# Kernel optimization log

Hardware: AMD Instinct MI355X
Metric: run time of the kernel (lower is better)

The kernel has to match this reference:

```python
import jax, jax.numpy as jnp
import numpy as np

B, H, S, D = 4, 16, 2048, 64

def setup_inputs() -> dict:
    key = jax.random.key(0)
    kq, kk, kv = jax.random.split(key, 3)
    q = jax.random.normal(kq, (B, H, S, D), dtype=jnp.float32)
    k = jax.random.normal(kk, (B, H, S, D), dtype=jnp.float32)
    v = jax.random.normal(kv, (B, H, S, D), dtype=jnp.float32)
    return {"q": q, "k": k, "v": v}

def reference(q, k, v):
    # Faithful port of TransformerBlock.scaled_dot_product_attention
    # (is_causal=True, mha_dropout=0.0 / eval mode).
    head_dim = q.shape[-1]
    scale = jnp.asarray(head_dim, q.dtype) ** -0.5
    q_len, k_len = q.shape[-2], k.shape[-2]
    # causal additive bias: 0 on/below diagonal, -inf above
    causal = jnp.tril(jnp.ones((q_len, k_len), dtype=bool))
    attn_bias = jnp.where(causal, jnp.asarray(0.0, q.dtype), jnp.asarray(-jnp.inf, q.dtype))
    # [b,h,s,d] x [b,h,t,d] -> [b,h,s,t]
    attn_weights = jnp.einsum('bhsd,bhtd->bhst', q * scale, k) + attn_bias
    attn = jax.nn.softmax(attn_weights, axis=-1)
    out = jnp.einsum('bhst,bhtd->bhsd', attn, v)
    return out
```

## Files before the change

### kernel.cpp

```cpp
#include <hip/hip_runtime.h>
#include <math.h>


#define S_LEN 2048
#define D_DIM 64
#define TK 64
#define NHEAD 64
#define MASKV -30000.0f
#define MINIT 1000.0f
#define DEFER_THR 12.0f
#define MNEG -30000.0f
#define LSTR 72
#define PREP_KBLK 4096

typedef __attribute__((ext_vector_type(8))) short bf16x8;
typedef __attribute__((ext_vector_type(4))) float f32x4;

static __device__ __forceinline__ float fast_exp2(float x) {
#if __has_builtin(__builtin_amdgcn_exp2f)
    return __builtin_amdgcn_exp2f(x);
#else
    float r;
    asm volatile("v_exp_f32 %0, %1\n\ts_nop 1" : "=v"(r) : "v"(x));
    return r;
#endif
}

static __device__ __forceinline__ float fmax3(float a, float b, float c) {
    return fmaxf(fmaxf(a, b), c);
}

static __device__ __forceinline__ unsigned int pack_bf16(float a, float b) {
    union { float f; unsigned int u; } ca, cb;
    ca.f = a; cb.f = b;
    unsigned int ua = ca.u + 0x8000u;
    unsigned int ub = cb.u + 0x8000u;
    return (ua >> 16) | (ub & 0xFFFF0000u);
}

static __device__ __forceinline__ unsigned int pack_bf16_fast(float a, float b) {
#if __has_builtin(__builtin_amdgcn_perm)
    union { float f; unsigned int u; } ca, cb;
    ca.f = a; cb.f = b;
    return __builtin_amdgcn_perm(cb.u + 0x8000u, ca.u + 0x8000u, 0x07060302u);
#else
    return pack_bf16(a, b);
#endif
}

typedef const __attribute__((address_space(1))) unsigned int* gas1_t;
typedef __attribute__((address_space(3))) unsigned int* las3_t;
static __device__ __forceinline__ void stage16(const void* g, void* l) {
    __builtin_amdgcn_global_load_lds((gas1_t)g, (las3_t)l, 16, 0, 0);
}

__global__ __launch_bounds__(256)
void fa_prep(const float* __restrict__ kg, const float* __restrict__ vg,
             unsigned short* __restrict__ kb, unsigned short* __restrict__ vb)
{
    const int tid = threadIdx.x;
    const int bid = blockIdx.x;
    if (bid < PREP_KBLK) {
        const int cid = bid * 256 + tid;
        const int ch  = cid & 7;
        const int row = cid >> 3;
        const int kv  = row & (S_LEN - 1);
        const float4* s = reinterpret_cast<const float4*>(kg + (size_t)row * D_DIM + ch * 8);
        float4 a = s[0], b = s[1];
        uint4 w;
        w.x = pack_bf16(a.x, a.y); w.y = pack_bf16(a.z, a.w);
        w.z = pack_bf16(b.x, b.y); w.w = pack_bf16(b.z, b.w);
        const int dst = ch ^ (kv & 7);
        *reinterpret_cast<uint4*>(kb + (size_t)row * D_DIM + dst * 8) = w;
    } else {
        const int wv   = (bid - PREP_KBLK) * 4 + (tid >> 6);
        const int lane = tid & 63;
        const int kg8  = lane >> 3;
        const int dg   = lane & 7;
        const float* s = vg + ((size_t)wv * TK + kg8 * 8) * D_DIM + dg * 8;
        float va[8][8];
        #pragma unroll
        for (int i = 0; i < 8; ++i) {
            const float4* sp = reinterpret_cast<const float4*>(s + (size_t)i * D_DIM);
            float4 x = sp[0], y = sp[1];
            va[i][0] = x.x; va[i][1] = x.y; va[i][2] = x.z; va[i][3] = x.w;
            va[i][4] = y.x; va[i][5] = y.y; va[i][6] = y.z; va[i][7] = y.w;
        }
        unsigned short* db = vb + (size_t)wv * (TK * D_DIM);
        #pragma unroll
        for (int j = 0; j < 8; ++j) {
            const int d = dg * 8 + j;
            uint4 w;
            w.x = pack_bf16(va[0][j], va[1][j]);
            w.y = pack_bf16(va[2][j], va[3][j]);
            w.z = pack_bf16(va[4][j], va[5][j]);
            w.w = pack_bf16(va[6][j], va[7][j]);
            *reinterpret_cast<uint4*>(db + d * D_DIM + 8 * (kg8 ^ j)) = w;
        }
    }
}

#define SOFTMAX_GROUP(SV, MC, LI, PL)                                          \
    {                                                                          \
        float x0 = fmax3(SV[0][0], SV[0][1], SV[0][2]);                        \
        float x1 = fmax3(SV[0][3], SV[1][0], SV[1][1]);                        \
        float x2 = fmax3(SV[1][2], SV[1][3], SV[2][0]);                        \
        float x3 = fmax3(SV[2][1], SV[2][2], SV[2][3]);                        \
        float x4 = fmax3(SV[3][0], SV[3][1], SV[3][2]);                        \
        float y0 = fmax3(x0, x1, x2);                                          \
        float y1 = fmax3(x3, x4, SV[3][3]);                                    \
        float rm = fmaxf(y0, y1);                                              \
        rm = fmaxf(rm, __shfl_xor(rm, 16, 64));                                \
        rm = fmaxf(rm, __shfl_xor(rm, 32, 64));                                \
        if (__any(rm > DEFER_THR)) {                                           \
            float mx    = fmaxf(rm, 0.f);                                      \
            float alpha = fast_exp2(-mx);                                      \
            LI *= alpha;                                                       \
            _Pragma("unroll")                                                  \
            for (int nc = 0; nc < 4; ++nc)                                     \
                _Pragma("unroll")                                              \
                for (int r = 0; r < 4; ++r) oacc##SV[nc][r] *= alpha;          \
            _Pragma("unroll")                                                  \
            for (int nt = 0; nt < 4; ++nt)                                     \
                _Pragma("unroll")                                              \
                for (int r = 0; r < 4; ++r) SV[nt][r] -= mx;                   \
            _Pragma("unroll")                                                  \
            for (int r = 0; r < 4; ++r) MC[r] -= mx;                           \
        }                                                                      \
        float rs = 0.f;                                                        \
        _Pragma("unroll")                                                      \
        for (int nt = 0; nt < 4; ++nt) {                                       \
            float e0 = fast_exp2(SV[nt][0]);                                   \
            float e1 = fast_exp2(SV[nt][1]);                                   \
            float e2 = fast_exp2(SV[nt][2]);                                   \
            float e3 = fast_exp2(SV[nt][3]);                                   \
            rs += (e0 + e1) + (e2 + e3);                                       \
            uint2 pw;                                                          \
            pw.x = pack_bf16_fast(e0, e1);                                     \
            pw.y = pack_bf16_fast(e2, e3);                                     \
            *reinterpret_cast<uint2*>(PL + ((nt * 32 + quad * 8) ^ swz)) = pw; \
        }                                                                      \
        rs += __shfl_xor(rs, 16, 64);                                          \
        rs += __shfl_xor(rs, 32, 64);                                          \
        LI += rs;                                                              \
    }

__global__ __launch_bounds__(256, 2)
void fa_fwd(const float* __restrict__ qg,
            const unsigned short* __restrict__ kb,
            const unsigned short* __restrict__ vb,
            float* __restrict__ og)
{
    const int head = blockIdx.x;
    const int pr   = blockIdx.y;
    const int tid  = threadIdx.x;
    const int wave = tid >> 6;
    const int lane = tid & 63;
    const int m16  = lane & 15;
    const int quad = lane >> 4;

    __shared__ unsigned short Kl[2][TK * D_DIM];
    __shared__ unsigned short Vt[2][TK * D_DIM];
    __shared__ unsigned short Pl[4][2][16 * TK];

    const size_t hoff = (size_t)head * S_LEN * D_DIM;
    const unsigned short* kbh = kb + hoff;
    const unsigned short* vbh = vb + hoff;
    float* __restrict__ ogh = og + hoff;

    const int swz  = (m16 & 7) << 4;
    const int colA = (quad * 16) ^ swz;
    const int colB = (64 + quad * 16) ^ swz;
    const int rowB = m16 * 128;
    const int sgo  = wave * 512 + lane * 8;

    char* klds = (char*)&Kl[0][0];
    char* vlds = (char*)&Vt[0][0];
    char* plA  = (char*)&Pl[0][0][0] + wave * 4096 + m16 * 128;
    char* plB  = plA + 2048;
    char* kw   = klds + wave * 1024;
    char* vw   = vlds + wave * 1024;

    const float QSC = 0.18033688011112042f;

    for (int pass = 0; pass < 2; ++pass) {
        const int idx = (pass == 0) ? pr : (15 - pr);
        const int q0  = idx * 128;
        const int T   = (q0 >> 6) + 1;

        bf16x8 qfA[2], qfB[2];
        {
            const float* qpA = qg + hoff + (size_t)(q0 + wave * 16 + m16) * D_DIM + quad * 8;
            #pragma unroll
            for (int c = 0; c < 2; ++c) {
                float4 a = reinterpret_cast<const float4*>(qpA + c * 32)[0];
                float4 b = reinterpret_cast<const float4*>(qpA + c * 32)[1];
                unsigned int u0 = pack_bf16(a.x * QSC, a.y * QSC);
                unsigned int u1 = pack_bf16(a.z * QSC, a.w * QSC);
                unsigned int u2 = pack_bf16(b.x * QSC, b.y * QSC);
                unsigned int u3 = pack_bf16(b.z * QSC, b.w * QSC);
                qfA[c][0] = (short)(u0 & 0xFFFF); qfA[c][1] = (short)(u0 >> 16);
                qfA[c][2] = (short)(u1 & 0xFFFF); qfA[c][3] = (short)(u1 >> 16);
                qfA[c][4] = (short)(u2 & 0xFFFF); qfA[c][5] = (short)(u2 >> 16);
                qfA[c][6] = (short)(u3 & 0xFFFF); qfA[c][7] = (short)(u3 >> 16);
            }
            const float* qpB = qpA + 64 * D_DIM;
            #pragma unroll
            for (int c = 0; c < 2; ++c) {
                float4 a = reinterpret_cast<const float4*>(qpB + c * 32)[0];
                float4 b = reinterpret_cast<const float4*>(qpB + c * 32)[1];
                unsigned int u0 = pack_bf16(a.x * QSC, a.y * QSC);
                unsigned int u1 = pack_bf16(a.z * QSC, a.w * QSC);
                unsigned int u2 = pack_bf16(b.x * QSC, b.y * QSC);
                unsigned int u3 = pack_bf16(b.z * QSC, b.w * QSC);
                qfB[c][0] = (short)(u0 & 0xFFFF); qfB[c][1] = (short)(u0 >> 16);
                qfB[c][2] = (short)(u1 & 0xFFFF); qfB[c][3] = (short)(u1 >> 16);
                qfB[c][4] = (short)(u2 & 0xFFFF); qfB[c][5] = (short)(u2 >> 16);
                qfB[c][6] = (short)(u3 & 0xFFFF); qfB[c][7] = (short)(u3 >> 16);
            }
        }

        float lA = 0.f, lB = 0.f;
        f32x4 mcA = (f32x4){MINIT, MINIT, MINIT, MINIT};
        f32x4 mcB = (f32x4){MINIT, MINIT, MINIT, MINIT};
        f32x4 oaccsvA[4], oaccsvB[4];
        #pragma unroll
        for (int nc = 0; nc < 4; ++nc) {
            oaccsvA[nc] = (f32x4){0.f, 0.f, 0.f, 0.f};
            oaccsvB[nc] = (f32x4){0.f, 0.f, 0.f, 0.f};
        }

        {
            const unsigned short* ks = kbh + sgo;
            const unsigned short* vs = vbh + sgo;
            stage16(ks,        kw);
            stage16(ks + 2048, kw + 4096);
            stage16(vs,        vw);
            stage16(vs + 2048, vw + 4096);
        }
        __syncthreads();

        int cur = 0;
        for (int t = 0; t <= T; ++t) {
            if (t < T) {
                const unsigned short* ks = kbh + (size_t)(t + 1) * 4096 + sgo;
                const unsigned short* vs = vbh + (size_t)(t + 1) * 4096 + sgo;
                const int nb = (cur ^ 1) * 8192;
                stage16(ks,        kw + nb);
                stage16(ks + 2048, kw + nb + 4096);
                stage16(vs,        vw + nb);
                stage16(vs + 2048, vw + nb + 4096);
            }

            const char* kt = klds + cur * 8192;
            const char* vt = vlds + cur * 8192;

            float svA[4][4], svB[4][4];
            __builtin_amdgcn_s_setprio(1);
            #pragma unroll
            for (int nt = 0; nt < 4; ++nt) {
                const char* kr = kt + nt * 2048 + rowB;
                bf16x8 kf0 = *reinterpret_cast<const bf16x8*>(kr + colA);
                bf16x8 kf1 = *reinterpret_cast<const bf16x8*>(kr + colB);
                f32x4 aA = __builtin_amdgcn_mfma_f32_16x16x32_bf16(kf0, qfA[0], mcA, 0, 0, 0);
                aA = __builtin_amdgcn_mfma_f32_16x16x32_bf16(kf1, qfA[1], aA, 0, 0, 0);
                f32x4 aB = __builtin_amdgcn_mfma_f32_16x16x32_bf16(kf0, qfB[0], mcB, 0, 0, 0);
                aB = __builtin_amdgcn_mfma_f32_16x16x32_bf16(kf1, qfB[1], aB, 0, 0, 0);
                #pragma unroll
                for (int r = 0; r < 4; ++r) { svA[nt][r] = aA[r]; svB[nt][r] = aB[r]; }
            }
            __builtin_amdgcn_s_setprio(0);

            if (t >= T - 1) {
                const int sh = (t - (T - 1)) << 6;
                #pragma unroll
                for (int nt = 0; nt < 4; ++nt)
                    #pragma unroll
                    for (int r = 0; r < 4; ++r)
                        if (sh + nt * 16 + quad * 4 + r > wave * 16 + m16) svA[nt][r] = MASKV;
            }
            if (t == T) {
                #pragma unroll
                for (int nt = 0; nt < 4; ++nt)
                    #pragma unroll
                    for (int r = 0; r < 4; ++r)
                        if (nt * 16 + quad * 4 + r > wave * 16 + m16) svB[nt][r] = MASKV;
            }

            SOFTMAX_GROUP(svA, mcA, lA, plA)
            SOFTMAX_GROUP(svB, mcB, lB, plB)

            asm volatile("s_waitcnt lgkmcnt(0)" ::: "memory");

            bf16x8 pfA0 = *reinterpret_cast<const bf16x8*>(plA + colA);
            bf16x8 pfA1 = *reinterpret_cast<const bf16x8*>(plA + colB);
            bf16x8 pfB0 = *reinterpret_cast<const bf16x8*>(plB + colA);
            bf16x8 pfB1 = *reinterpret_cast<const bf16x8*>(plB + colB);
            __builtin_amdgcn_s_setprio(1);
            #pragma unroll
            for (int nc = 0; nc < 4; ++nc) {
                const char* vr = vt + nc * 2048 + rowB;
                bf16x8 vf0 = *reinterpret_cast<const bf16x8*>(vr + colA);
                bf16x8 vf1 = *reinterpret_cast<const bf16x8*>(vr + colB);
                oaccsvA[nc] = __builtin_amdgcn_mfma_f32_16x16x32_bf16(vf0, pfA0, oaccsvA[nc], 0, 0, 0);
                oaccsvA[nc] = __builtin_amdgcn_mfma_f32_16x16x32_bf16(vf1, pfA1, oaccsvA[nc], 0, 0, 0);
                oaccsvB[nc] = __builtin_amdgcn_mfma_f32_16x16x32_bf16(vf0, pfB0, oaccsvB[nc], 0, 0, 0);
                oaccsvB[nc] = __builtin_amdgcn_mfma_f32_16x16x32_bf16(vf1, pfB1, oaccsvB[nc], 0, 0, 0);
            }
            __builtin_amdgcn_s_setprio(0);

            __syncthreads();
            cur ^= 1;
        }

        {
            float inv = 1.0f / lA;
            float* op = ogh + (size_t)(q0 + wave * 16 + m16) * D_DIM;
            #pragma unroll
            for (int nc = 0; nc < 4; ++nc) {
                float4 o4;
                o4.x = oaccsvA[nc][0] * inv;
                o4.y = oaccsvA[nc][1] * inv;
                o4.z = oaccsvA[nc][2] * inv;
                o4.w = oaccsvA[nc][3] * inv;
                reinterpret_cast<float4*>(op + nc * 16 + quad * 4)[0] = o4;
            }
        }
        {
            float inv = 1.0f / lB;
            float* op = ogh + (size_t)(q0 + 64 + wave * 16 + m16) * D_DIM;
            #pragma unroll
            for (int nc = 0; nc < 4; ++nc) {
                float4 o4;
                o4.x = oaccsvB[nc][0] * inv;
                o4.y = oaccsvB[nc][1] * inv;
                o4.z = oaccsvB[nc][2] * inv;
                o4.w = oaccsvB[nc][3] * inv;
                reinterpret_cast<float4*>(op + nc * 16 + quad * 4)[0] = o4;
            }
        }
    }
}

__global__ __launch_bounds__(256, 4)
void fa_fwd_fb(const float* __restrict__ qg,
               const float* __restrict__ kg,
               const float* __restrict__ vg,
               float* __restrict__ og)
{
    const int head = blockIdx.x;
    const int pr   = blockIdx.y;
    const int tid  = threadIdx.x;
    const int wave = tid >> 6;
    const int lane = tid & 63;
    const int m16  = lane & 15;
    const int quad = lane >> 4;

    __shared__ unsigned short Kl[TK][LSTR];
    __shared__ unsigned short Vt[D_DIM][LSTR];
    __shared__ unsigned short Pl[4][16][LSTR];

    const size_t hoff = (size_t)head * S_LEN * D_DIM;
    const float* kh = kg + hoff;
    const float* vh = vg + hoff;

    const int ksr = tid >> 2;
    const int ksc = (tid & 3) << 4;
    const int va  = lane >> 3;
    const int vb  = lane & 7;
    const int vrr = wave * 16 + 2 * vb;
    const int vcc = 8 * va;
    const float LOG2E = 1.4426950408889634f;

    for (int pass = 0; pass < 2; ++pass) {
        const int q0 = ((pass == 0) ? pr : (31 - pr)) * TK;

        bf16x8 qf[2];
        {
            const float* qp = qg + hoff + (size_t)(q0 + wave * 16 + m16) * D_DIM + quad * 8;
            #pragma unroll
            for (int c = 0; c < 2; ++c) {
                float4 a = reinterpret_cast<const float4*>(qp + c * 32)[0];
                float4 b = reinterpret_cast<const float4*>(qp + c * 32)[1];
                unsigned int u0 = pack_bf16(a.x * 0.125f, a.y * 0.125f);
                unsigned int u1 = pack_bf16(a.z * 0.125f, a.w * 0.125f);
                unsigned int u2 = pack_bf16(b.x * 0.125f, b.y * 0.125f);
                unsigned int u3 = pack_bf16(b.z * 0.125f, b.w * 0.125f);
                qf[c][0] = (short)(u0 & 0xFFFF); qf[c][1] = (short)(u0 >> 16);
                qf[c][2] = (short)(u1 & 0xFFFF); qf[c][3] = (short)(u1 >> 16);
                qf[c][4] = (short)(u2 & 0xFFFF); qf[c][5] = (short)(u2 >> 16);
                qf[c][6] = (short)(u3 & 0xFFFF); qf[c][7] = (short)(u3 >> 16);
            }
        }

        float m_i = MNEG, l_i = 0.f;
        f32x4 oacc[4];
        #pragma unroll
        for (int nc = 0; nc < 4; ++nc) oacc[nc] = (f32x4){0.f, 0.f, 0.f, 0.f};

        float4 kA, kB, kC, kD, vA, vB, vC, vD;
        {
            const float* kp = kh + (size_t)ksr * D_DIM + ksc;
            kA = reinterpret_cast<const float4*>(kp)[0];
            kB = reinterpret_cast<const float4*>(kp)[1];
            kC = reinterpret_cast<const float4*>(kp)[2];
            kD = reinterpret_cast<const float4*>(kp)[3];
            const float* vp = vh + (size_t)vrr * D_DIM + vcc;
            vA = reinterpret_cast<const float4*>(vp)[0];
            vB = reinterpret_cast<const float4*>(vp)[1];
            vC = reinterpret_cast<const float4*>(vp + D_DIM)[0];
            vD = reinterpret_cast<const float4*>(vp + D_DIM)[1];
        }

        for (int j0 = 0; j0 <= q0; j0 += TK) {
            __syncthreads();
            {
                uint4 w0, w1;
                w0.x = pack_bf16(kA.x, kA.y); w0.y = pack_bf16(kA.z, kA.w);
                w0.z = pack_bf16(kB.x, kB.y); w0.w = pack_bf16(kB.z, kB.w);
                w1.x = pack_bf16(kC.x, kC.y); w1.y = pack_bf16(kC.z, kC.w);
                w1.z = pack_bf16(kD.x, kD.y); w1.w = pack_bf16(kD.z, kD.w);
                *reinterpret_cast<uint4*>(&Kl[ksr][ksc])     = w0;
                *reinterpret_cast<uint4*>(&Kl[ksr][ksc + 8]) = w1;

                float r0[8] = {vA.x, vA.y, vA.z, vA.w, vB.x, vB.y, vB.z, vB.w};
                float r1[8] = {vC.x, vC.y, vC.z, vC.w, vD.x, vD.y, vD.z, vD.w};
                #pragma unroll
                for (int jj = 0; jj < 8; ++jj) {
                    int j = (jj + va) & 7;
                    *reinterpret_cast<unsigned int*>(&Vt[vcc + j][vrr]) = pack_bf16(r0[j], r1[j]);
                }
            }
            __syncthreads();

            if (j0 + TK <= q0) {
                const float* kp = kh + (size_t)(j0 + TK + ksr) * D_DIM + ksc;
                kA = reinterpret_cast<const float4*>(kp)[0];
                kB = reinterpret_cast<const float4*>(kp)[1];
                kC = reinterpret_cast<const float4*>(kp)[2];
                kD = reinterpret_cast<const float4*>(kp)[3];
                const float* vp = vh + (size_t)(j0 + TK + vrr) * D_DIM + vcc;
                vA = reinterpret_cast<const float4*>(vp)[0];
                vB = reinterpret_cast<const float4*>(vp)[1];
                vC = reinterpret_cast<const float4*>(vp + D_DIM)[0];
                vD = reinterpret_cast<const float4*>(vp + D_DIM)[1];
            }

            float sv[4][4];
            #pragma unroll
            for (int nt = 0; nt < 4; ++nt) {
                f32x4 acc = (f32x4){0.f, 0.f, 0.f, 0.f};
                bf16x8 kf0 = *reinterpret_cast<const bf16x8*>(&Kl[nt * 16 + m16][quad * 8]);
                bf16x8 kf1 = *reinterpret_cast<const bf16x8*>(&Kl[nt * 16 + m16][32 + quad * 8]);
                acc = __builtin_amdgcn_mfma_f32_16x16x32_bf16(kf0, qf[0], acc, 0, 0, 0);
                acc = __builtin_amdgcn_mfma_f32_16x16x32_bf16(kf1, qf[1], acc, 0, 0, 0);
                #pragma unroll
                for (int r = 0; r < 4; ++r) sv[nt][r] = acc[r];
            }

            if (j0 == q0) {
                #pragma unroll
                for (int nt = 0; nt < 4; ++nt)
                    #pragma unroll
                    for (int r = 0; r < 4; ++r)
                        if (nt * 16 + quad * 4 + r > wave * 16 + m16) sv[nt][r] = MNEG;
            }

            float a0 = fmaxf(fmaxf(sv[0][0], sv[0][1]), fmaxf(sv[0][2], sv[0][3]));
            float a1 = fmaxf(fmaxf(sv[1][0], sv[1][1]), fmaxf(sv[1][2], sv[1][3]));
            float a2 = fmaxf(fmaxf(sv[2][0], sv[2][1]), fmaxf(sv[2][2], sv[2][3]));
            float a3 = fmaxf(fmaxf(sv[3][0], sv[3][1]), fmaxf(sv[3][2], sv[3][3]));
            float rm = fmaxf(fmaxf(a0, a1), fmaxf(a2, a3));
            rm = fmaxf(rm, __shfl_xor(rm, 16, 64));
            rm = fmaxf(rm, __shfl_xor(rm, 32, 64));
            float mnew  = fmaxf(m_i, rm);
            float alpha = fast_exp2((m_i - mnew) * LOG2E);
            float msc   = mnew * LOG2E;
            m_i = mnew;

            float rs = 0.f;
            #pragma unroll
            for (int nt = 0; nt < 4; ++nt) {
                float e0 = fast_exp2(fmaf(sv[nt][0], LOG2E, -msc));
                float e1 = fast_exp2(fmaf(sv[nt][1], LOG2E, -msc));
                float e2 = fast_exp2(fmaf(sv[nt][2], LOG2E, -msc));
                float e3 = fast_exp2(fmaf(sv[nt][3], LOG2E, -msc));
                rs += (e0 + e1) + (e2 + e3);
                uint2 pw;
                pw.x = pack_bf16(e0, e1);
                pw.y = pack_bf16(e2, e3);
                *reinterpret_cast<uint2*>(&Pl[wave][m16][nt * 16 + quad * 4]) = pw;
            }
            rs += __shfl_xor(rs, 16, 64);
            rs += __shfl_xor(rs, 32, 64);
            l_i = fmaf(alpha, l_i, rs);

            #pragma unroll
            for (int nc = 0; nc < 4; ++nc)
                #pragma unroll
                for (int r = 0; r < 4; ++r)
                    oacc[nc][r] *= alpha;

            asm volatile("s_waitcnt lgkmcnt(0)" ::: "memory");

            bf16x8 pf0 = *reinterpret_cast<const bf16x8*>(&Pl[wave][m16][quad * 8]);
            bf16x8 pf1 = *reinterpret_cast<const bf16x8*>(&Pl[wave][m16][32 + quad * 8]);
            #pragma unroll
            for (int nc = 0; nc < 4; ++nc) {
                bf16x8 vf0 = *reinterpret_cast<const bf16x8*>(&Vt[nc * 16 + m16][quad * 8]);
                bf16x8 vf1 = *reinterpret_cast<const bf16x8*>(&Vt[nc * 16 + m16][32 + quad * 8]);
                oacc[nc] = __builtin_amdgcn_mfma_f32_16x16x32_bf16(vf0, pf0, oacc[nc], 0, 0, 0);
                oacc[nc] = __builtin_amdgcn_mfma_f32_16x16x32_bf16(vf1, pf1, oacc[nc], 0, 0, 0);
            }
        }

        float inv = 1.0f / l_i;
        float* op = og + hoff + (size_t)(q0 + wave * 16 + m16) * D_DIM;
        #pragma unroll
        for (int nc = 0; nc < 4; ++nc) {
            float4 o4;
            o4.x = oacc[nc][0] * inv;
            o4.y = oacc[nc][1] * inv;
            o4.z = oacc[nc][2] * inv;
            o4.w = oacc[nc][3] * inv;
            reinterpret_cast<float4*>(op + nc * 16 + quad * 4)[0] = o4;
        }
    }
}

extern "C" void kernel_launch(void* const* d_in, const int* in_sizes, int n_in,
                              void* d_out, int out_size, void* d_ws, size_t ws_size,
                              hipStream_t stream) {
    const float* q = (const float*)d_in[0];
    const float* k = (const float*)d_in[1];
    const float* v = (const float*)d_in[2];
    float* o = (float*)d_out;
    const size_t kvShorts = (size_t)NHEAD * S_LEN * D_DIM;
    const size_t wsNeed   = 2 * kvShorts * sizeof(unsigned short);
    if (d_ws != nullptr && ws_size >= wsNeed) {
        unsigned short* kb = (unsigned short*)d_ws;
        unsigned short* vb = kb + kvShorts;
        fa_prep<<<PREP_KBLK + 512, 256, 0, stream>>>(k, v, kb, vb);
        dim3 grid(NHEAD, 8);
        fa_fwd<<<grid, 256, 0, stream>>>(q, kb, vb, o);
    } else {
        dim3 grid(NHEAD, 16);
        fa_fwd_fb<<<grid, 256, 0, stream>>>(q, k, v, o);
    }
}
```

Measured before the change: 200.9 us.

## Software-pipeline QK of next tile with triple-buffered K/V staging

K/V shared-memory staging goes from double to triple buffering, and K/V is prefetched two tiles ahead. The QK MFMA for tile t+1 is issued before the softmax and PV of tile t, so matrix work can overlap the exp/max VALU work. Score tiles are kept in two alternating register sets, and the deferred max rescale also shifts the already-computed next tile. The cost is more LDS per block and more VGPRs, which may cause spills or lower occupancy.

```diff
diff --git a/kernel.cpp b/kernel.cpp
--- a/kernel.cpp
+++ b/kernel.cpp
@@ -100,7 +100,58 @@
     }
 }
 
-#define SOFTMAX_GROUP(SV, MC, LI, PL)                                          \
+#define STAGE(TI)                                                              \
+    {                                                                          \
+        const int b_ = (TI) % 3;                                               \
+        const unsigned short* ks_ = kbh + (size_t)(TI) * 4096 + sgo;           \
+        const unsigned short* vs_ = vbh + (size_t)(TI) * 4096 + sgo;           \
+        char* kd_ = klds + b_ * 8192 + wave * 1024;                            \
+        char* vd_ = vlds + b_ * 8192 + wave * 1024;                            \
+        stage16(ks_,        kd_);                                              \
+        stage16(ks_ + 2048, kd_ + 4096);                                       \
+        stage16(vs_,        vd_);                                              \
+        stage16(vs_ + 2048, vd_ + 4096);                                       \
+    }
+
+#define QK_TILE(BUFI, SVA, SVB)                                                \
+    {                                                                          \
+        const char* kt_ = klds + (BUFI) * 8192;                                \
+        __builtin_amdgcn_s_setprio(1);                                         \
+        _Pragma("unroll")                                                      \
+        for (int nt = 0; nt < 4; ++nt) {                                       \
+            const char* kr_ = kt_ + nt * 2048 + rowB;                          \
+            bf16x8 kf0 = *reinterpret_cast<const bf16x8*>(kr_ + colA);         \
+            bf16x8 kf1 = *reinterpret_cast<const bf16x8*>(kr_ + colB);         \
+            f32x4 aA = __builtin_amdgcn_mfma_f32_16x16x32_bf16(kf0, qfA[0], mcA, 0, 0, 0); \
+            aA = __builtin_amdgcn_mfma_f32_16x16x32_bf16(kf1, qfA[1], aA, 0, 0, 0);        \
+            f32x4 aB = __builtin_amdgcn_mfma_f32_16x16x32_bf16(kf0, qfB[0], mcB, 0, 0, 0); \
+            aB = __builtin_amdgcn_mfma_f32_16x16x32_bf16(kf1, qfB[1], aB, 0, 0, 0);        \
+            _Pragma("unroll")                                                  \
+            for (int r = 0; r < 4; ++r) { SVA[nt][r] = aA[r]; SVB[nt][r] = aB[r]; } \
+        }                                                                      \
+        __builtin_amdgcn_s_setprio(0);                                         \
+    }
+
+#define MASK_TILES(U, SVA, SVB)                                                \
+    {                                                                          \
+        if ((U) >= T - 1) {                                                    \
+            const int sh_ = ((U) - (T - 1)) << 6;                              \
+            _Pragma("unroll")                                                  \
+            for (int nt = 0; nt < 4; ++nt)                                     \
+                _Pragma("unroll")                                              \
+                for (int r = 0; r < 4; ++r)                                    \
+                    if (sh_ + nt * 16 + quad * 4 + r > wave * 16 + m16) SVA[nt][r] = MASKV; \
+        }                                                                      \
+        if ((U) == T) {                                                        \
+            _Pragma("unroll")                                                  \
+            for (int nt = 0; nt < 4; ++nt)                                     \
+                _Pragma("unroll")                                              \
+                for (int r = 0; r < 4; ++r)                                    \
+                    if (nt * 16 + quad * 4 + r > wave * 16 + m16) SVB[nt][r] = MASKV; \
+        }                                                                      \
+    }
+
+#define SOFTMAX_G(SV, SVN, MC, LI, OACC, PL)                                   \
     {                                                                          \
         float x0 = fmax3(SV[0][0], SV[0][1], SV[0][2]);                        \
         float x1 = fmax3(SV[0][3], SV[1][0], SV[1][1]);                        \
@@ -119,11 +170,11 @@
             _Pragma("unroll")                                                  \
             for (int nc = 0; nc < 4; ++nc)                                     \
                 _Pragma("unroll")                                              \
-                for (int r = 0; r < 4; ++r) oacc##SV[nc][r] *= alpha;          \
+                for (int r = 0; r < 4; ++r) OACC[nc][r] *= alpha;              \
             _Pragma("unroll")                                                  \
             for (int nt = 0; nt < 4; ++nt)                                     \
                 _Pragma("unroll")                                              \
-                for (int r = 0; r < 4; ++r) SV[nt][r] -= mx;                   \
+                for (int r = 0; r < 4; ++r) { SV[nt][r] -= mx; SVN[nt][r] -= mx; } \
             _Pragma("unroll")                                                  \
             for (int r = 0; r < 4; ++r) MC[r] -= mx;                           \
         }                                                                      \
@@ -143,6 +194,38 @@
         rs += __shfl_xor(rs, 16, 64);                                          \
         rs += __shfl_xor(rs, 32, 64);                                          \
         LI += rs;                                                              \
+    }
+
+#define FA_STEP(TT, SCA, SCB, SNA, SNB)                                        \
+    {                                                                          \
+        if ((TT) + 2 <= T) STAGE((TT) + 2);                                    \
+        if ((TT) + 1 <= T) {                                                   \
+            QK_TILE(((TT) + 1) % 3, SNA, SNB);                                 \
+            MASK_TILES((TT) + 1, SNA, SNB);                                    \
+        }                                                                      \
+        SOFTMAX_G(SCA, SNA, mcA, lA, oaccA, plA);                              \
+        SOFTMAX_G(SCB, SNB, mcB, lB, oaccB, plB);                              \
+        asm volatile("s_waitcnt lgkmcnt(0)" ::: "memory");                     \
+        {                                                                      \
+            const char* vt_ = vlds + ((TT) % 3) * 8192;                        \
+            bf16x8 pfA0 = *reinterpret_cast<const bf16x8*>(plA + colA);        \
+            bf16x8 pfA1 = *reinterpret_cast<const bf16x8*>(plA + colB);        \
+            bf16x8 pfB0 = *reinterpret_cast<const bf16x8*>(plB + colA);        \
+            bf16x8 pfB1 = *reinterpret_cast<const bf16x8*>(plB + colB);        \
+            __builtin_amdgcn_s_setprio(1);                                     \
+            _Pragma("unroll")                                                  \
+            for (int nc = 0; nc < 4; ++nc) {                                   \
+                const char* vr_ = vt_ + nc * 2048 + rowB;                      \
+                bf16x8 vf0 = *reinterpret_cast<const bf16x8*>(vr_ + colA);     \
+                bf16x8 vf1 = *reinterpret_cast<const bf16x8*>(vr_ + colB);     \
+                oaccA[nc] = __builtin_amdgcn_mfma_f32_16x16x32_bf16(vf0, pfA0, oaccA[nc], 0, 0, 0); \
+                oaccA[nc] = __builtin_amdgcn_mfma_f32_16x16x32_bf16(vf1, pfA1, oaccA[nc], 0, 0, 0); \
+                oaccB[nc] = __builtin_amdgcn_mfma_f32_16x16x32_bf16(vf0, pfB0, oaccB[nc], 0, 0, 0); \
+                oaccB[nc] = __builtin_amdgcn_mfma_f32_16x16x32_bf16(vf1, pfB1, oaccB[nc], 0, 0, 0); \
+            }                                                                  \
+            __builtin_amdgcn_s_setprio(0);                                     \
+        }                                                                      \
+        __syncthreads();                                                       \
     }
 
 __global__ __launch_bounds__(256, 2)
@@ -159,8 +242,8 @@
     const int m16  = lane & 15;
     const int quad = lane >> 4;
 
-    __shared__ unsigned short Kl[2][TK * D_DIM];
-    __shared__ unsigned short Vt[2][TK * D_DIM];
+    __shared__ unsigned short Kl[3][TK * D_DIM];
+    __shared__ unsigned short Vt[3][TK * D_DIM];
     __shared__ unsigned short Pl[4][2][16 * TK];
 
     const size_t hoff = (size_t)head * S_LEN * D_DIM;
@@ -178,8 +261,6 @@
     char* vlds = (char*)&Vt[0][0];
     char* plA  = (char*)&Pl[0][0][0] + wave * 4096 + m16 * 128;
     char* plB  = plA + 2048;
-    char* kw   = klds + wave * 1024;
-    char* vw   = vlds + wave * 1024;
 
     const float QSC = 0.18033688011112042f;
 
@@ -223,94 +304,24 @@
         float lA = 0.f, lB = 0.f;
         f32x4 mcA = (f32x4){MINIT, MINIT, MINIT, MINIT};
         f32x4 mcB = (f32x4){MINIT, MINIT, MINIT, MINIT};
-        f32x4 oaccsvA[4], oaccsvB[4];
+        f32x4 oaccA[4], oaccB[4];
         #pragma unroll
         for (int nc = 0; nc < 4; ++nc) {
-            oaccsvA[nc] = (f32x4){0.f, 0.f, 0.f, 0.f};
-            oaccsvB[nc] = (f32x4){0.f, 0.f, 0.f, 0.f};
-        }
-
-        {
-            const unsigned short* ks = kbh + sgo;
-            const unsigned short* vs = vbh + sgo;
-            stage16(ks,        kw);
-            stage16(ks + 2048, kw + 4096);
-            stage16(vs,        vw);
-            stage16(vs + 2048, vw + 4096);
-        }
+            oaccA[nc] = (f32x4){0.f, 0.f, 0.f, 0.f};
+            oaccB[nc] = (f32x4){0.f, 0.f, 0.f, 0.f};
+        }
+
+        STAGE(0)
+        STAGE(1)
         __syncthreads();
 
-        int cur = 0;
-        for (int t = 0; t <= T; ++t) {
-            if (t < T) {
-                const unsigned short* ks = kbh + (size_t)(t + 1) * 4096 + sgo;
-                const unsigned short* vs = vbh + (size_t)(t + 1) * 4096 + sgo;
-                const int nb = (cur ^ 1) * 8192;
-                stage16(ks,        kw + nb);
-                stage16(ks + 2048, kw + nb + 4096);
-                stage16(vs,        vw + nb);
-                stage16(vs + 2048, vw + nb + 4096);
-            }
-
-            const char* kt = klds + cur * 8192;
-            const char* vt = vlds + cur * 8192;
-
-            float svA[4][4], svB[4][4];
-            __builtin_amdgcn_s_setprio(1);
-            #pragma unroll
-            for (int nt = 0; nt < 4; ++nt) {
-                const char* kr = kt + nt * 2048 + rowB;
-                bf16x8 kf0 = *reinterpret_cast<const bf16x8*>(kr + colA);
-                bf16x8 kf1 = *reinterpret_cast<const bf16x8*>(kr + colB);
-                f32x4 aA = __builtin_amdgcn_mfma_f32_16x16x32_bf16(kf0, qfA[0], mcA, 0, 0, 0);
-                aA = __builtin_amdgcn_mfma_f32_16x16x32_bf16(kf1, qfA[1], aA, 0, 0, 0);
-                f32x4 aB = __builtin_amdgcn_mfma_f32_16x16x32_bf16(kf0, qfB[0], mcB, 0, 0, 0);
-                aB = __builtin_amdgcn_mfma_f32_16x16x32_bf16(kf1, qfB[1], aB, 0, 0, 0);
-                #pragma unroll
-                for (int r = 0; r < 4; ++r) { svA[nt][r] = aA[r]; svB[nt][r] = aB[r]; }
-            }
-            __builtin_amdgcn_s_setprio(0);
-
-            if (t >= T - 1) {
-                const int sh = (t - (T - 1)) << 6;
-                #pragma unroll
-                for (int nt = 0; nt < 4; ++nt)
-                    #pragma unroll
-                    for (int r = 0; r < 4; ++r)
-                        if (sh + nt * 16 + quad * 4 + r > wave * 16 + m16) svA[nt][r] = MASKV;
-            }
-            if (t == T) {
-                #pragma unroll
-                for (int nt = 0; nt < 4; ++nt)
-                    #pragma unroll
-                    for (int r = 0; r < 4; ++r)
-                        if (nt * 16 + quad * 4 + r > wave * 16 + m16) svB[nt][r] = MASKV;
-            }
-
-            SOFTMAX_GROUP(svA, mcA, lA, plA)
-            SOFTMAX_GROUP(svB, mcB, lB, plB)
-
-            asm volatile("s_waitcnt lgkmcnt(0)" ::: "memory");
-
-            bf16x8 pfA0 = *reinterpret_cast<const bf16x8*>(plA + colA);
-            bf16x8 pfA1 = *reinterpret_cast<const bf16x8*>(plA + colB);
-            bf16x8 pfB0 = *reinterpret_cast<const bf16x8*>(plB + colA);
-            bf16x8 pfB1 = *reinterpret_cast<const bf16x8*>(plB + colB);
-            __builtin_amdgcn_s_setprio(1);
-            #pragma unroll
-            for (int nc = 0; nc < 4; ++nc) {
-                const char* vr = vt + nc * 2048 + rowB;
-                bf16x8 vf0 = *reinterpret_cast<const bf16x8*>(vr + colA);
-                bf16x8 vf1 = *reinterpret_cast<const bf16x8*>(vr + colB);
-                oaccsvA[nc] = __builtin_amdgcn_mfma_f32_16x16x32_bf16(vf0, pfA0, oaccsvA[nc], 0, 0, 0);
-                oaccsvA[nc] = __builtin_amdgcn_mfma_f32_16x16x32_bf16(vf1, pfA1, oaccsvA[nc], 0, 0, 0);
-                oaccsvB[nc] = __builtin_amdgcn_mfma_f32_16x16x32_bf16(vf0, pfB0, oaccsvB[nc], 0, 0, 0);
-                oaccsvB[nc] = __builtin_amdgcn_mfma_f32_16x16x32_bf16(vf1, pfB1, oaccsvB[nc], 0, 0, 0);
-            }
-            __builtin_amdgcn_s_setprio(0);
-
-            __syncthreads();
-            cur ^= 1;
+        float svcA[4][4], svcB[4][4], svnA[4][4], svnB[4][4];
+        QK_TILE(0, svcA, svcB)
+        MASK_TILES(0, svcA, svcB)
+
+        for (int t = 0; t <= T; t += 2) {
+            FA_STEP(t,     svcA, svcB, svnA, svnB)
+            FA_STEP(t + 1, svnA, svnB, svcA, svcB)
         }
 
         {
@@ -319,10 +330,10 @@
             #pragma unroll
             for (int nc = 0; nc < 4; ++nc) {
                 float4 o4;
-                o4.x = oaccsvA[nc][0] * inv;
-                o4.y = oaccsvA[nc][1] * inv;
-                o4.z = oaccsvA[nc][2] * inv;
-                o4.w = oaccsvA[nc][3] * inv;
+                o4.x = oaccA[nc][0] * inv;
+                o4.y = oaccA[nc][1] * inv;
+                o4.z = oaccA[nc][2] * inv;
+                o4.w = oaccA[nc][3] * inv;
                 reinterpret_cast<float4*>(op + nc * 16 + quad * 4)[0] = o4;
             }
         }
@@ -332,10 +343,10 @@
             #pragma unroll
             for (int nc = 0; nc < 4; ++nc) {
                 float4 o4;
-                o4.x = oaccsvB[nc][0] * inv;
-                o4.y = oaccsvB[nc][1] * inv;
-                o4.z = oaccsvB[nc][2] * inv;
-                o4.w = oaccsvB[nc][3] * inv;
+                o4.x = oaccB[nc][0] * inv;
+                o4.y = oaccB[nc][1] * inv;
+                o4.z = oaccB[nc][2] * inv;
+                o4.w = oaccB[nc][3] * inv;
                 reinterpret_cast<float4*>(op + nc * 16 + quad * 4)[0] = o4;
             }
         }
```

Measured after the change: 203.8 us. Within noise of the previous version (+1.4%).
